# Kernel optimization log

Hardware: AMD Instinct MI355X
Metric: run time of the kernel (lower is better)

## Reference

```python
import jax, jax.numpy as jnp
import numpy as np

B, T, H, V, S = 32, 1024, 512, 1024, 128
PAD = 0          # PAD_token, also the CTC blank
NEG = -1e30      # finite stand-in for -inf (grad-safe)


def setup_inputs() -> dict:
    key = jax.random.key(0)
    ks = jax.random.split(key, 5)
    padded_input = jax.random.normal(ks[0], (B, T, H), dtype=jnp.float32)
    # labels in [1, V) so no PAD inside targets -> target_lengths == S
    padded_target = jax.random.randint(ks[1], (B, S), 1, V).astype(jnp.int32)
    input_lengths = jax.random.randint(ks[2], (B,), T // 2, T + 1).astype(jnp.int32)
    W1 = jax.random.normal(ks[3], (H, H), dtype=jnp.float32) * 0.02
    b1 = jnp.zeros((H,), jnp.float32)
    W2 = jax.random.normal(ks[4], (H, V), dtype=jnp.float32) * 0.02
    b2 = jnp.zeros((V,), jnp.float32)
    return {"padded_target": padded_target, "padded_input": padded_input,
            "input_lengths": input_lengths, "W1": W1, "b1": b1, "W2": W2, "b2": b2}


def _ctc_loss(log_probs, targets, input_lengths, target_lengths, blank=PAD):
    """CTC negative log-likelihood per example (reduction='none').
    log_probs: [B,T,V] (log-softmaxed), targets: [B,S] int."""
    Bb, Tt, _ = log_probs.shape
    Ss = targets.shape[1]
    L = 2 * Ss + 1  # extended label sequence: blank,y1,blank,...,yS,blank
    ext = jnp.full((Bb, L), blank, dtype=targets.dtype).at[:, 1::2].set(targets)
    # gather log-probs of extended labels: [B,T,L] -> [T,B,L]
    lp_ext = jnp.take_along_axis(
        log_probs, jnp.broadcast_to(ext[:, None, :], (Bb, Tt, L)), axis=2)
    lp_ext = jnp.transpose(lp_ext, (1, 0, 2))
    # skip transition (s-2 -> s) allowed when ext[s] != blank and ext[s] != ext[s-2]
    skip = jnp.concatenate(
        [jnp.zeros((Bb, 2), bool),
         (ext[:, 2:] != blank) & (ext[:, 2:] != ext[:, :-2])], axis=1)

    alpha0 = jnp.full((Bb, L), NEG, jnp.float32)
    alpha0 = alpha0.at[:, 0].set(lp_ext[0, :, 0]).at[:, 1].set(lp_ext[0, :, 1])

    def step(alpha, xs):
        lp_t, t = xs
        s1 = jnp.concatenate([jnp.full((Bb, 1), NEG, jnp.float32), alpha[:, :-1]], axis=1)
        s2 = jnp.concatenate([jnp.full((Bb, 2), NEG, jnp.float32), alpha[:, :-2]], axis=1)
        a = jnp.logaddexp(alpha, s1)
        a = jnp.where(skip, jnp.logaddexp(a, s2), a)
        new = a + lp_t
        # freeze alpha past each example's input length
        new = jnp.where((t < input_lengths)[:, None], new, alpha)
        return new, None

    alpha, _ = jax.lax.scan(step, alpha0, (lp_ext[1:], jnp.arange(1, Tt)))
    end1 = jnp.take_along_axis(alpha, (2 * target_lengths - 1)[:, None], axis=1)[:, 0]
    end2 = jnp.take_along_axis(alpha, (2 * target_lengths)[:, None], axis=1)[:, 0]
    return -jnp.logaddexp(end1, end2)


def reference(padded_target, padded_input, input_lengths, W1, b1, W2, b2):
    target_lengths = jnp.sum(padded_target != PAD, axis=1).astype(jnp.int32)
    h = jnp.tanh(padded_input @ W1 + b1)          # [B,T,H]
    logits = h @ W2 + b2                           # [B,T,V]
    log_probs = jax.nn.log_softmax(logits, axis=-1)
    loss = _ctc_loss(log_probs, padded_target, input_lengths, target_lengths)
    return loss / target_lengths.astype(jnp.float32)  # [B]
```

## Files before the change

kernel.cpp:

```cpp
#include <hip/hip_runtime.h>
#include <hip/hip_bf16.h>
#include <math.h>

#define Bq 32
#define Tt 1024
#define Hh 512
#define Vv 1024
#define Ss 128

typedef short bf16x8 __attribute__((ext_vector_type(8)));
typedef float f32x4 __attribute__((ext_vector_type(4)));

#define GLDS(srcp, dstp, sz) \
  __builtin_amdgcn_global_load_lds( \
      (const __attribute__((address_space(1))) void*)(srcp), \
      (__attribute__((address_space(3))) void*)(dstp), sz, 0, 0)

__device__ __forceinline__ ushort f2bf(float v) {
  __hip_bfloat16 hv = __float2bfloat16(v);
  return *(ushort*)&hv;
}

template <int N>
__device__ __forceinline__ void wb() {
  __asm__ volatile("s_waitcnt vmcnt(%0)" ::"i"(N) : "memory");
  __builtin_amdgcn_s_barrier();
}

#define BFLY_ADD(v) { \
  v += __int_as_float(__builtin_amdgcn_ds_swizzle(__float_as_int(v), 0x041F)); \
  v += __int_as_float(__builtin_amdgcn_ds_swizzle(__float_as_int(v), 0x081F)); \
  v += __int_as_float(__builtin_amdgcn_ds_swizzle(__float_as_int(v), 0x101F)); \
  v += __int_as_float(__builtin_amdgcn_ds_swizzle(__float_as_int(v), 0x201F)); }

__global__ void transpose_cvt2(const float* __restrict__ W1, const float* __restrict__ W2,
                               ushort* __restrict__ W1T, ushort* __restrict__ W2T) {
  __shared__ float tile[32][33];
  const int bid = blockIdx.x;
  const float* in; ushort* out; int K, N, bx, by;
  if (bid < 256) { in = W1; out = W1T; K = Hh; N = Hh; bx = bid & 15; by = bid >> 4; }
  else { const int b2 = bid - 256; in = W2; out = W2T; K = Hh; N = Vv; bx = b2 & 31; by = b2 >> 5; }
  const int k0 = by * 32, n0 = bx * 32;
  const int tx = threadIdx.x, ty = threadIdx.y;
  for (int i = ty; i < 32; i += 8)
    tile[i][tx] = in[(size_t)(k0 + i) * N + n0 + tx];
  __syncthreads();
  for (int i = ty; i < 32; i += 8)
    out[(size_t)(n0 + i) * K + k0 + tx] = f2bf(tile[tx][i]);
}

__global__ __launch_bounds__(256, 2)
void gemm1_fused(const float* __restrict__ X, const ushort* __restrict__ Bt,
                 const float* __restrict__ bias, const int* __restrict__ lens,
                 ushort* __restrict__ H) {
  __shared__ ushort Bs[4][128 * 64];
  const int row0 = blockIdx.x * 64;
  if ((row0 & (Tt - 1)) >= lens[blockIdx.x >> 4]) return;

  const int tid = threadIdx.x;
  const int lane = tid & 63, wave = tid >> 6;
  const int wm = wave >> 1, wn = wave & 1;
  const int q = lane >> 4, r16 = lane & 15;
  const int lrow = lane >> 3;
  const int swz = (lane & 7) ^ lrow;
  const int rx = r16 & 7;
  const int kx0 = (q ^ rx) * 8;
  const int kx1 = ((4 + q) ^ rx) * 8;

  float bcolAll[4][4];
#pragma unroll
  for (int nt = 0; nt < 4; ++nt)
#pragma unroll
    for (int ni = 0; ni < 4; ++ni)
      bcolAll[nt][ni] = bias[nt * 128 + wn * 64 + ni * 16 + r16];

  bf16x8 af[16][2];
#pragma unroll
  for (int ks = 0; ks < 16; ++ks)
#pragma unroll
    for (int mi = 0; mi < 2; ++mi) {
      const float* src = X + (size_t)(row0 + wm * 32 + mi * 16 + r16) * Hh + ks * 32 + q * 8;
      const float4 f0 = *(const float4*)(src);
      const float4 f1 = *(const float4*)(src + 4);
      union { bf16x8 v; ushort u[8]; } pk;
      pk.u[0] = f2bf(f0.x); pk.u[1] = f2bf(f0.y); pk.u[2] = f2bf(f0.z); pk.u[3] = f2bf(f0.w);
      pk.u[4] = f2bf(f1.x); pk.u[5] = f2bf(f1.y); pk.u[6] = f2bf(f1.z); pk.u[7] = f2bf(f1.w);
      af[ks][mi] = pk.v;
    }

  auto stageF = [&](int nt2, int kc2, int d2) {
#pragma unroll
    for (int i = 0; i < 4; ++i) {
      const int seg = wave * 4 + i;
      const int rr = seg * 8 + lrow;
      GLDS(Bt + (size_t)(nt2 * 128 + rr) * Hh + kc2 * 64 + swz * 8, &Bs[d2][seg * 512], 16);
    }
  };
  auto readFrags = [&](bf16x8 (&bfr)[2][4], int d) {
#pragma unroll
    for (int ni = 0; ni < 4; ++ni) {
      bfr[0][ni] = *(const bf16x8*)(&Bs[d][((wn * 64 + ni * 16 + r16) << 6) + kx0]);
      bfr[1][ni] = *(const bf16x8*)(&Bs[d][((wn * 64 + ni * 16 + r16) << 6) + kx1]);
    }
  };

  stageF(0, 0, 0);
  stageF(0, 1, 1);
  wb<4>();
  bf16x8 bcur[2][4], bnxt[2][4];
  readFrags(bcur, 0);

  f32x4 acc[2][4];
#pragma unroll
  for (int i = 0; i < 2; ++i)
#pragma unroll
    for (int j = 0; j < 4; ++j) acc[i][j] = (f32x4){0.f, 0.f, 0.f, 0.f};

  for (int nt = 0; nt < 4; ++nt) {
#pragma unroll
    for (int kc = 0; kc < 8; ++kc) {
      const bool haveS = !(nt == 3 && kc >= 6);
      const bool haveN = !(nt == 3 && kc == 7);
      if (haveS) stageF(nt + (kc >= 6 ? 1 : 0), (kc + 2) & 7, (kc + 2) & 3);
      if (haveN) {
        if (haveS) wb<4>(); else wb<0>();
        readFrags(bnxt, (kc + 1) & 3);
      }
#pragma unroll
      for (int ksl = 0; ksl < 2; ++ksl)
#pragma unroll
        for (int mi = 0; mi < 2; ++mi)
#pragma unroll
          for (int ni = 0; ni < 4; ++ni)
            acc[mi][ni] = __builtin_amdgcn_mfma_f32_16x16x32_bf16(af[kc * 2 + ksl][mi], bcur[ksl][ni], acc[mi][ni], 0, 0, 0);
#pragma unroll
      for (int z = 0; z < 2; ++z)
#pragma unroll
        for (int ni = 0; ni < 4; ++ni) bcur[z][ni] = bnxt[z][ni];
      if (kc == 7) {
#pragma unroll
        for (int mi = 0; mi < 2; ++mi)
#pragma unroll
          for (int r = 0; r < 4; ++r) {
            const int row = row0 + wm * 32 + mi * 16 + q * 4 + r;
#pragma unroll
            for (int ni = 0; ni < 4; ++ni) {
              const float v = acc[mi][ni][r] + bcolAll[nt][ni];
              const float ex = __expf(2.0f * v);
              const float th = (ex - 1.0f) / (ex + 1.0f);
              H[(size_t)row * Hh + nt * 128 + wn * 64 + ni * 16 + r16] = f2bf(th);
            }
            acc[mi][0][r] = 0.f; acc[mi][1][r] = 0.f; acc[mi][2][r] = 0.f; acc[mi][3][r] = 0.f;
          }
      }
    }
  }
}

__global__ __launch_bounds__(256, 2)
void gemm2sm(const ushort* __restrict__ Aq, const ushort* __restrict__ Bt,
             const float* __restrict__ bias, const int* __restrict__ tgt,
             const int* __restrict__ lens,
             ushort* __restrict__ pOdd, ushort* __restrict__ pBlank) {
  __shared__ ushort Bs[4][128 * 64];
  __shared__ float biasLds[Vv];
  __shared__ int tgLds[128];
  __shared__ float blankL[64];
  __shared__ float rowSum[64];
  __shared__ float tmpP[2][64];

  const int row0 = blockIdx.x * 64;
  const int bEx = blockIdx.x >> 4;
  if ((row0 & (Tt - 1)) >= lens[bEx]) return;

  const int tid = threadIdx.x;
  const int lane = tid & 63, wave = tid >> 6;
  const int wm = wave >> 1, wn = wave & 1;
  const int q = lane >> 4, r16 = lane & 15;
  const int lrow = lane >> 3;
  const int swz = (lane & 7) ^ lrow;
  const int rx = r16 & 7;
  const int kx0 = (q ^ rx) * 8;
  const int kx1 = ((4 + q) ^ rx) * 8;

  bf16x8 af[16][2];
#pragma unroll
  for (int ks = 0; ks < 16; ++ks)
#pragma unroll
    for (int mi = 0; mi < 2; ++mi)
      af[ks][mi] = *(const bf16x8*)(Aq + (size_t)(row0 + wm * 32 + mi * 16 + r16) * Hh + ks * 32 + q * 8);

  GLDS(bias + tid * 4, (char*)biasLds + wave * 1024, 16);
  if (tid < 128) tgLds[tid] = tgt[bEx * Ss + tid];

  auto stageF = [&](int nt2, int kc2, int d2) {
#pragma unroll
    for (int i = 0; i < 4; ++i) {
      const int seg = wave * 4 + i;
      const int rr = seg * 8 + lrow;
      const ushort* src = (nt2 < 8)
          ? Bt + (size_t)(nt2 * 128 + rr) * Hh + kc2 * 64 + swz * 8
          : Bt + (size_t)tgLds[rr] * Hh + kc2 * 64 + swz * 8;
      GLDS(src, &Bs[d2][seg * 512], 16);
    }
  };
  auto readFrags = [&](bf16x8 (&bfr)[2][4], int d) {
#pragma unroll
    for (int ni = 0; ni < 4; ++ni) {
      bfr[0][ni] = *(const bf16x8*)(&Bs[d][((wn * 64 + ni * 16 + r16) << 6) + kx0]);
      bfr[1][ni] = *(const bf16x8*)(&Bs[d][((wn * 64 + ni * 16 + r16) << 6) + kx1]);
    }
  };

  stageF(0, 0, 0);
  stageF(0, 1, 1);
  __asm__ volatile("s_waitcnt lgkmcnt(0)" ::: "memory");
  wb<4>();
  bf16x8 bcur[2][4], bnxt[2][4];
  readFrags(bcur, 0);

  f32x4 acc[2][4];
#pragma unroll
  for (int i = 0; i < 2; ++i)
#pragma unroll
    for (int j = 0; j < 4; ++j) acc[i][j] = (f32x4){0.f, 0.f, 0.f, 0.f};
  float rowP[2][4] = {{0.f, 0.f, 0.f, 0.f}, {0.f, 0.f, 0.f, 0.f}};

  for (int nt = 0; nt < 9; ++nt) {
#pragma unroll
    for (int kc = 0; kc < 8; ++kc) {
      const bool haveS = !(nt == 8 && kc >= 6);
      const bool haveN = !(nt == 8 && kc == 7);
      if (haveS) stageF(nt + (kc >= 6 ? 1 : 0), (kc + 2) & 7, (kc + 2) & 3);
      if (haveN) {
        if (haveS) wb<4>(); else wb<0>();
        readFrags(bnxt, (kc + 1) & 3);
      }
#pragma unroll
      for (int ksl = 0; ksl < 2; ++ksl)
#pragma unroll
        for (int mi = 0; mi < 2; ++mi)
#pragma unroll
          for (int ni = 0; ni < 4; ++ni)
            acc[mi][ni] = __builtin_amdgcn_mfma_f32_16x16x32_bf16(af[kc * 2 + ksl][mi], bcur[ksl][ni], acc[mi][ni], 0, 0, 0);
#pragma unroll
      for (int z = 0; z < 2; ++z)
#pragma unroll
        for (int ni = 0; ni < 4; ++ni) bcur[z][ni] = bnxt[z][ni];

      if (kc == 7) {
        if (nt < 8) {
          float bcol[4];
#pragma unroll
          for (int ni = 0; ni < 4; ++ni) bcol[ni] = biasLds[nt * 128 + wn * 64 + ni * 16 + r16];
          if (nt == 0 && wn == 0 && r16 == 0) {
#pragma unroll
            for (int mi = 0; mi < 2; ++mi)
#pragma unroll
              for (int r = 0; r < 4; ++r)
                blankL[wm * 32 + mi * 16 + q * 4 + r] = acc[mi][0][r] + bcol[0];
          }
#pragma unroll
          for (int mi = 0; mi < 2; ++mi)
#pragma unroll
            for (int r = 0; r < 4; ++r) {
              float s = __expf(acc[mi][0][r] + bcol[0]);
              s += __expf(acc[mi][1][r] + bcol[1]);
              s += __expf(acc[mi][2][r] + bcol[2]);
              s += __expf(acc[mi][3][r] + bcol[3]);
              rowP[mi][r] += s;
              acc[mi][0][r] = 0.f; acc[mi][1][r] = 0.f; acc[mi][2][r] = 0.f; acc[mi][3][r] = 0.f;
            }
          if (nt == 7) {
            float sred[2][4];
#pragma unroll
            for (int mi = 0; mi < 2; ++mi)
#pragma unroll
              for (int r = 0; r < 4; ++r) {
                float s = rowP[mi][r];
                BFLY_ADD(s);
                sred[mi][r] = s;
              }
            if (r16 == 0) {
#pragma unroll
              for (int mi = 0; mi < 2; ++mi) {
                float4 w = {sred[mi][0], sred[mi][1], sred[mi][2], sred[mi][3]};
                *(float4*)&tmpP[wn][wm * 32 + mi * 16 + q * 4] = w;
              }
            }
            __syncthreads();
            if (tid < 64) {
              const float tot = tmpP[0][tid] + tmpP[1][tid];
              rowSum[tid] = tot;
              pBlank[row0 + tid] = f2bf(__expf(blankL[tid]) * 64.0f / tot);
            }
            __syncthreads();
          }
        } else {
          float bcl[4];
#pragma unroll
          for (int ni = 0; ni < 4; ++ni) bcl[ni] = biasLds[tgLds[wn * 64 + ni * 16 + r16]];
#pragma unroll
          for (int mi = 0; mi < 2; ++mi) {
            const float4 rs4 = *(const float4*)&rowSum[wm * 32 + mi * 16 + q * 4];
#pragma unroll
            for (int r = 0; r < 4; ++r) {
              const float sc = 64.0f / ((const float*)&rs4)[r];
              const int row = row0 + wm * 32 + mi * 16 + q * 4 + r;
#pragma unroll
              for (int ni = 0; ni < 4; ++ni) {
                const float p = __expf(acc[mi][ni][r] + bcl[ni]) * sc;
                pOdd[(size_t)row * Ss + wn * 64 + ni * 16 + r16] = f2bf(p);
              }
            }
          }
        }
      }
    }
  }
}

__device__ __forceinline__ float dpp_wshr1(float x) {
  return __int_as_float(__builtin_amdgcn_update_dpp(
      0, __float_as_int(x), 0x138, 0xf, 0xf, true));
}
__device__ __forceinline__ float dpp_wave_max(float m) {
  m = fmaxf(m, __int_as_float(__builtin_amdgcn_update_dpp(0, __float_as_int(m), 0x111, 0xf, 0xf, true)));
  m = fmaxf(m, __int_as_float(__builtin_amdgcn_update_dpp(0, __float_as_int(m), 0x112, 0xf, 0xf, true)));
  m = fmaxf(m, __int_as_float(__builtin_amdgcn_update_dpp(0, __float_as_int(m), 0x114, 0xf, 0xf, true)));
  m = fmaxf(m, __int_as_float(__builtin_amdgcn_update_dpp(0, __float_as_int(m), 0x118, 0xf, 0xf, true)));
  m = fmaxf(m, __int_as_float(__builtin_amdgcn_update_dpp(__float_as_int(m), __float_as_int(m), 0x142, 0xf, 0xf, false)));
  m = fmaxf(m, __int_as_float(__builtin_amdgcn_update_dpp(__float_as_int(m), __float_as_int(m), 0x143, 0xf, 0xf, false)));
  return __int_as_float(__builtin_amdgcn_readlane(__float_as_int(m), 63));
}

__global__ __launch_bounds__(64)
void ctc_dp(const ushort* __restrict__ pOddG, const ushort* __restrict__ pBlankG,
            const int* __restrict__ tgt, const int* __restrict__ lens,
            float* __restrict__ out) {
  __shared__ ushort pO[2][72 * 128];
  __shared__ ushort pBl[2][128];
  const int b = blockIdx.x, l = threadIdx.x;
  const ushort* pObase = pOddG + (size_t)b * Tt * Ss;
  const ushort* pBbase = pBlankG + (size_t)b * Tt;
  const int* tg = tgt + b * Ss;
  const int len = lens[b];

  float sk1 = 0.f, sk3;
  if (l >= 1) sk1 = (tg[2 * l] != tg[2 * l - 1]) ? 1.f : 0.f;
  sk3 = (tg[2 * l + 1] != tg[2 * l]) ? 1.f : 0.f;

  auto stage = [&](int c, int d) {
    const ushort* src = pObase + (size_t)c * 64 * 128;
#pragma unroll
    for (int i = 0; i < 16; ++i)
      GLDS(src + (i * 64 + l) * 8, &pO[d][i * 512], 16);
    GLDS(pBbase + c * 64 + l * 2, &pBl[d][0], 4);
  };

  stage(0, 0);
  __syncthreads();

  float a0 = 0.f, a1 = 0.f, a2 = 0.f, a3 = 0.f, a4 = 0.f;
  if (l == 0) {
    a0 = __int_as_float(((unsigned)pBl[0][0]) << 16);
    a1 = __int_as_float(((unsigned)pO[0][0]) << 16);
  }
  int E = 0;

  auto renorm = [&]() {
    float m = fmaxf(fmaxf(fmaxf(a0, a1), fmaxf(a2, a3)), a4);
    const float gm = dpp_wave_max(m);
    const int e = (int)((__float_as_uint(gm) >> 23) & 255) - 127;
    int sh = 30 - e; if (sh > 120) sh = 120;
    const float scale = __uint_as_float((unsigned)(127 + sh) << 23);
    E -= sh;
    a0 *= scale; a1 *= scale; a2 *= scale; a3 *= scale; a4 *= scale;
  };

  auto run_dyn = [&](int d, int stA, int stB, int tbase) {
    const int n = stB - stA;
    if (n <= 0) return;
    unsigned qL[4], qB[4];
#pragma unroll
    for (int k = 0; k < 4; ++k) {
      const int st = stA + k;
      qL[k] = *(const unsigned*)&pO[d][(st << 7) + 2 * l];
      qB[k] = (unsigned)pBl[d][st];
    }
    auto body = [&](int i, int k) {
      const float pOa = __int_as_float(qL[k] << 16);
      const float pObv = __int_as_float(qL[k] & 0xffff0000u);
      const float pB = __int_as_float(qB[k] << 16);
      const float h3 = dpp_wshr1(a3);
      const float n0 = (a0 + h3) * pB;
      const float n1 = fmaf(sk1, h3, a1 + a0) * pOa;
      const float n2 = (a2 + a1) * pB;
      const float n3 = fmaf(sk3, a1, a3 + a2) * pObv;
      const float n4 = (a4 + a3) * pB;
      a0 = n0; a1 = n1; a2 = n2; a3 = n3; a4 = n4;
      const int st2 = stA + i + 4;
      qL[k] = *(const unsigned*)&pO[d][(st2 << 7) + 2 * l];
      qB[k] = (unsigned)pBl[d][st2];
      if (((tbase + i) & 7) == 0) renorm();
    };
    int i = 0;
    for (; i + 4 <= n; i += 4) { body(i, 0); body(i + 1, 1); body(i + 2, 2); body(i + 3, 3); }
    if ((n & 3) > 0) body(i, 0);
    if ((n & 3) > 1) body(i + 1, 1);
    if ((n & 3) > 2) body(i + 2, 2);
  };

  auto run_full = [&](int d) {
    unsigned qL[8], qB[4];
#pragma unroll
    for (int k = 0; k < 8; ++k)
      qL[k] = *(const unsigned*)&pO[d][(k << 7) + 2 * l];
#pragma unroll
    for (int j = 0; j < 4; ++j)
      qB[j] = *(const unsigned*)&pBl[d][2 * j];
    for (int i = 0; i < 64; i += 8) {
#pragma unroll
      for (int k = 0; k < 8; ++k) {
        const float pOa = __int_as_float(qL[k] << 16);
        const float pObv = __int_as_float(qL[k] & 0xffff0000u);
        const unsigned bb = qB[k >> 1];
        const float pB = __int_as_float((k & 1) ? (bb & 0xffff0000u) : (bb << 16));
        const float h3 = dpp_wshr1(a3);
        const float n0 = (a0 + h3) * pB;
        const float n1 = fmaf(sk1, h3, a1 + a0) * pOa;
        const float n2 = (a2 + a1) * pB;
        const float n3 = fmaf(sk3, a1, a3 + a2) * pObv;
        const float n4 = (a4 + a3) * pB;
        a0 = n0; a1 = n1; a2 = n2; a3 = n3; a4 = n4;
        qL[k] = *(const unsigned*)&pO[d][((i + k + 8) << 7) + 2 * l];
        if (k & 1) qB[k >> 1] = *(const unsigned*)&pBl[d][i + k + 7];
        if (k == 0) renorm();
      }
    }
  };

  if (64 < len) stage(1, 1);
  run_dyn(0, 1, (64 < len) ? 64 : len, 1);
  __syncthreads();
  const int Cfull = len >> 6;
  for (int c = 1; c < Cfull; ++c) {
    const int d = c & 1;
    if ((c + 1) * 64 < len) stage(c + 1, d ^ 1);
    run_full(d);
    __syncthreads();
  }
  if (len & 63) run_dyn(Cfull & 1, 0, len & 63, Cfull * 64);

  const int tl = __popcll(__ballot(tg[l] != 0)) + __popcll(__ballot(tg[64 + l] != 0));
  const int s1 = 2 * tl - 1, s2 = 2 * tl;
  float v = 0.f;
  const int sb = 4 * l;
  if (sb == s1 || sb == s2) v += a0;
  if (sb + 1 == s1 || sb + 1 == s2) v += a1;
  if (sb + 2 == s1 || sb + 2 == s2) v += a2;
  if (sb + 3 == s1 || sb + 3 == s2) v += a3;
  if (l == 63 && s2 == 256) v += a4;
#pragma unroll
  for (int off = 1; off < 64; off <<= 1) v += __shfl_xor(v, off);
  if (l == 0)
    out[b] = -((log2f(v) + (float)E - 6.0f * (float)len) * 0.6931471805599453f) / (float)tl;
}

extern "C" void kernel_launch(void* const* d_in, const int* in_sizes, int n_in,
                              void* d_out, int out_size, void* d_ws, size_t ws_size,
                              hipStream_t stream) {
  const int*   targets = (const int*)d_in[0];
  const float* X       = (const float*)d_in[1];
  const int*   lens    = (const int*)d_in[2];
  const float* W1      = (const float*)d_in[3];
  const float* b1      = (const float*)d_in[4];
  const float* W2      = (const float*)d_in[5];
  const float* b2      = (const float*)d_in[6];
  float* out = (float*)d_out;

  ushort* h       = (ushort*)d_ws;
  ushort* W1T     = h + (size_t)Bq * Tt * Hh;
  ushort* W2T     = W1T + (size_t)Hh * Hh;
  ushort* pOddG   = W2T + (size_t)Vv * Hh;
  ushort* pBlankG = pOddG + (size_t)Bq * Tt * Ss;

  transpose_cvt2<<<dim3(768), dim3(32, 8), 0, stream>>>(W1, W2, W1T, W2T);
  gemm1_fused<<<dim3((Bq * Tt) / 64), dim3(256), 0, stream>>>(X, W1T, b1, lens, h);
  gemm2sm<<<dim3((Bq * Tt) / 64), dim3(256), 0, stream>>>(h, W2T, b2, targets, lens, pOddG, pBlankG);
  ctc_dp<<<dim3(Bq), dim3(64), 0, stream>>>(pOddG, pBlankG, targets, lens, out);
}
```

Baseline: 236.2 us.

## Restructure GEMM B-staging into paired-chunk double buffering with fewer barriers

Both GEMM kernels now stage two K-chunks per step into a pair of LDS buffers and compute from the other pair, instead of a four-deep ring with one chunk per step and register prefetch of the next fragments. This halves the number of wait/barrier points per N tile and drops the register copy of prefetched fragments. In exchange, LDS reads are no longer overlapped with the previous step's MFMAs, so fragment-read latency may become exposed.

```diff
diff --git a/kernel.cpp b/kernel.cpp
--- a/kernel.cpp
+++ b/kernel.cpp
@@ -88,12 +88,12 @@
       af[ks][mi] = pk.v;
     }
 
-  auto stageF = [&](int nt2, int kc2, int d2) {
+  auto stageChunk = [&](int nt2, int kc2, int buf) {
 #pragma unroll
     for (int i = 0; i < 4; ++i) {
       const int seg = wave * 4 + i;
       const int rr = seg * 8 + lrow;
-      GLDS(Bt + (size_t)(nt2 * 128 + rr) * Hh + kc2 * 64 + swz * 8, &Bs[d2][seg * 512], 16);
+      GLDS(Bt + (size_t)(nt2 * 128 + rr) * Hh + kc2 * 64 + swz * 8, &Bs[buf][seg * 512], 16);
     }
   };
   auto readFrags = [&](bf16x8 (&bfr)[2][4], int d) {
@@ -104,11 +104,8 @@
     }
   };
 
-  stageF(0, 0, 0);
-  stageF(0, 1, 1);
-  wb<4>();
-  bf16x8 bcur[2][4], bnxt[2][4];
-  readFrags(bcur, 0);
+  stageChunk(0, 0, 0);
+  stageChunk(0, 1, 1);
 
   f32x4 acc[2][4];
 #pragma unroll
@@ -118,26 +115,37 @@
 
   for (int nt = 0; nt < 4; ++nt) {
 #pragma unroll
-    for (int kc = 0; kc < 8; ++kc) {
-      const bool haveS = !(nt == 3 && kc >= 6);
-      const bool haveN = !(nt == 3 && kc == 7);
-      if (haveS) stageF(nt + (kc >= 6 ? 1 : 0), (kc + 2) & 7, (kc + 2) & 3);
-      if (haveN) {
-        if (haveS) wb<4>(); else wb<0>();
-        readFrags(bnxt, (kc + 1) & 3);
+    for (int sc = 0; sc < 4; ++sc) {
+      const int p = sc & 1;
+      const int pn = (sc + 1) & 1;
+      const bool haveS = !(nt == 3 && sc == 3);
+      if (haveS) {
+        const int ntn = nt + (sc == 3 ? 1 : 0);
+        stageChunk(ntn, (2 * sc + 2) & 7, 2 * pn);
+        stageChunk(ntn, (2 * sc + 3) & 7, 2 * pn + 1);
+        wb<8>();
+      } else {
+        wb<0>();
       }
+      bf16x8 frA[2][4], frB[2][4];
+      readFrags(frA, 2 * p);
+      readFrags(frB, 2 * p + 1);
 #pragma unroll
       for (int ksl = 0; ksl < 2; ++ksl)
 #pragma unroll
         for (int mi = 0; mi < 2; ++mi)
 #pragma unroll
           for (int ni = 0; ni < 4; ++ni)
-            acc[mi][ni] = __builtin_amdgcn_mfma_f32_16x16x32_bf16(af[kc * 2 + ksl][mi], bcur[ksl][ni], acc[mi][ni], 0, 0, 0);
-#pragma unroll
-      for (int z = 0; z < 2; ++z)
-#pragma unroll
-        for (int ni = 0; ni < 4; ++ni) bcur[z][ni] = bnxt[z][ni];
-      if (kc == 7) {
+            acc[mi][ni] = __builtin_amdgcn_mfma_f32_16x16x32_bf16(af[4 * sc + ksl][mi], frA[ksl][ni], acc[mi][ni], 0, 0, 0);
+#pragma unroll
+      for (int ksl = 0; ksl < 2; ++ksl)
+#pragma unroll
+        for (int mi = 0; mi < 2; ++mi)
+#pragma unroll
+          for (int ni = 0; ni < 4; ++ni)
+            acc[mi][ni] = __builtin_amdgcn_mfma_f32_16x16x32_bf16(af[4 * sc + 2 + ksl][mi], frB[ksl][ni], acc[mi][ni], 0, 0, 0);
+
+      if (sc == 3) {
 #pragma unroll
         for (int mi = 0; mi < 2; ++mi)
 #pragma unroll
@@ -193,7 +201,7 @@
   GLDS(bias + tid * 4, (char*)biasLds + wave * 1024, 16);
   if (tid < 128) tgLds[tid] = tgt[bEx * Ss + tid];
 
-  auto stageF = [&](int nt2, int kc2, int d2) {
+  auto stageChunk = [&](int nt2, int kc2, int buf) {
 #pragma unroll
     for (int i = 0; i < 4; ++i) {
       const int seg = wave * 4 + i;
@@ -201,7 +209,7 @@
       const ushort* src = (nt2 < 8)
           ? Bt + (size_t)(nt2 * 128 + rr) * Hh + kc2 * 64 + swz * 8
           : Bt + (size_t)tgLds[rr] * Hh + kc2 * 64 + swz * 8;
-      GLDS(src, &Bs[d2][seg * 512], 16);
+      GLDS(src, &Bs[buf][seg * 512], 16);
     }
   };
   auto readFrags = [&](bf16x8 (&bfr)[2][4], int d) {
@@ -212,12 +220,9 @@
     }
   };
 
-  stageF(0, 0, 0);
-  stageF(0, 1, 1);
   __asm__ volatile("s_waitcnt lgkmcnt(0)" ::: "memory");
-  wb<4>();
-  bf16x8 bcur[2][4], bnxt[2][4];
-  readFrags(bcur, 0);
+  stageChunk(0, 0, 0);
+  stageChunk(0, 1, 1);
 
   f32x4 acc[2][4];
 #pragma unroll
@@ -228,27 +233,37 @@
 
   for (int nt = 0; nt < 9; ++nt) {
 #pragma unroll
-    for (int kc = 0; kc < 8; ++kc) {
-      const bool haveS = !(nt == 8 && kc >= 6);
-      const bool haveN = !(nt == 8 && kc == 7);
-      if (haveS) stageF(nt + (kc >= 6 ? 1 : 0), (kc + 2) & 7, (kc + 2) & 3);
-      if (haveN) {
-        if (haveS) wb<4>(); else wb<0>();
-        readFrags(bnxt, (kc + 1) & 3);
+    for (int sc = 0; sc < 4; ++sc) {
+      const int p = sc & 1;
+      const int pn = (sc + 1) & 1;
+      const bool haveS = !(nt == 8 && sc == 3);
+      if (haveS) {
+        const int ntn = nt + (sc == 3 ? 1 : 0);
+        stageChunk(ntn, (2 * sc + 2) & 7, 2 * pn);
+        stageChunk(ntn, (2 * sc + 3) & 7, 2 * pn + 1);
+        wb<8>();
+      } else {
+        wb<0>();
       }
+      bf16x8 frA[2][4], frB[2][4];
+      readFrags(frA, 2 * p);
+      readFrags(frB, 2 * p + 1);
 #pragma unroll
       for (int ksl = 0; ksl < 2; ++ksl)
 #pragma unroll
         for (int mi = 0; mi < 2; ++mi)
 #pragma unroll
           for (int ni = 0; ni < 4; ++ni)
-            acc[mi][ni] = __builtin_amdgcn_mfma_f32_16x16x32_bf16(af[kc * 2 + ksl][mi], bcur[ksl][ni], acc[mi][ni], 0, 0, 0);
-#pragma unroll
-      for (int z = 0; z < 2; ++z)
-#pragma unroll
-        for (int ni = 0; ni < 4; ++ni) bcur[z][ni] = bnxt[z][ni];
-
-      if (kc == 7) {
+            acc[mi][ni] = __builtin_amdgcn_mfma_f32_16x16x32_bf16(af[4 * sc + ksl][mi], frA[ksl][ni], acc[mi][ni], 0, 0, 0);
+#pragma unroll
+      for (int ksl = 0; ksl < 2; ++ksl)
+#pragma unroll
+        for (int mi = 0; mi < 2; ++mi)
+#pragma unroll
+          for (int ni = 0; ni < 4; ++ni)
+            acc[mi][ni] = __builtin_amdgcn_mfma_f32_16x16x32_bf16(af[4 * sc + 2 + ksl][mi], frB[ksl][ni], acc[mi][ni], 0, 0, 0);
+
+      if (sc == 3) {
         if (nt < 8) {
           float bcol[4];
 #pragma unroll
@@ -305,12 +320,12 @@
             const float4 rs4 = *(const float4*)&rowSum[wm * 32 + mi * 16 + q * 4];
 #pragma unroll
             for (int r = 0; r < 4; ++r) {
-              const float sc = 64.0f / ((const float*)&rs4)[r];
+              const float sc2 = 64.0f / ((const float*)&rs4)[r];
               const int row = row0 + wm * 32 + mi * 16 + q * 4 + r;
 #pragma unroll
               for (int ni = 0; ni < 4; ++ni) {
-                const float p = __expf(acc[mi][ni][r] + bcl[ni]) * sc;
-                pOdd[(size_t)row * Ss + wn * 64 + ni * 16 + r16] = f2bf(p);
+                const float pv = __expf(acc[mi][ni][r] + bcl[ni]) * sc2;
+                pOdd[(size_t)row * Ss + wn * 64 + ni * 16 + r16] = f2bf(pv);
               }
             }
           }
```

New measurement: 229.6 us. 2.8% less time.
